# Optimization experiments

Measured on AMD Instinct MI355X. Metric: run time of the kernel, lower is better.

Reference implementation:

```python
import jax, jax.numpy as jnp
import numpy as np

PARTIAL_DATA_THRESHOLD = 0.1  # threshold on squared NN distance (ChamferDistance returns squared dists)


def setup_inputs() -> dict:
    key = jax.random.key(0)
    k1, k2 = jax.random.split(key)
    scan_vertices = jax.random.normal(k1, (50000, 3), dtype=jnp.float32)      # N x 3
    template_vertices = jax.random.normal(k2, (6890, 3), dtype=jnp.float32)   # M x 3
    return {"scan_vertices": scan_vertices, "template_vertices": template_vertices}


def reference(scan_vertices, template_vertices):
    # Directional (template -> scan) Chamfer: for each template point, squared
    # distance to nearest scan point; then sum distances below threshold.
    # d2[m, n] = |t_m|^2 + |s_n|^2 - 2 t_m . s_n
    t_sq = jnp.sum(template_vertices * template_vertices, axis=-1)            # [M]
    s_sq = jnp.sum(scan_vertices * scan_vertices, axis=-1)                    # [N]
    cross = jnp.einsum('md,nd->mn', template_vertices, scan_vertices)         # [M, N]
    d2 = t_sq[:, None] + s_sq[None, :] - 2.0 * cross                          # [M, N]
    template2scan = jnp.min(d2, axis=1)                                       # [M]
    mask = template2scan < PARTIAL_DATA_THRESHOLD
    return jnp.sum(jnp.where(mask, template2scan, 0.0))
```

## Files before the change

### kernel.cpp

```cpp
#include <hip/hip_runtime.h>
#include <hip/hip_bf16.h>

#define BLK 256
#define SPLITS 24
#define FRTOT 1584
#define FPS (FRTOT / SPLITS)
#define NSLOT (FRTOT * 32)
#define THRESH 0.1f
#define KEY_MAX 0xFFFFFFFFu
#define ONE_BF ((unsigned short)0x3F80)

typedef __attribute__((ext_vector_type(8))) short short8;
typedef __attribute__((ext_vector_type(16))) float floatx16;

__device__ __forceinline__ unsigned short f2bf(float x) {
    unsigned u = __float_as_uint(x);
    unsigned r = u + 0x7FFFu + ((u >> 16) & 1u);
    return (unsigned short)(r >> 16);
}
__device__ __forceinline__ float bf2f(unsigned short h) {
    return __uint_as_float(((unsigned)h) << 16);
}

__device__ __forceinline__ unsigned f2key(float f) {
    unsigned b = __float_as_uint(f);
    return (b & 0x80000000u) ? ~b : (b | 0x80000000u);
}
__device__ __forceinline__ float key2f(unsigned k) {
    return __uint_as_float((k & 0x80000000u) ? (k & 0x7FFFFFFFu) : ~k);
}

template <int CTRL>
__device__ __forceinline__ float dpp_ror_min(float v) {
    const int i = __float_as_int(v);
    const int p = __builtin_amdgcn_update_dpp(i, i, CTRL, 0xF, 0xF, false);
    return fminf(v, __int_as_float(p));
}

__global__ __launch_bounds__(BLK) void pdl_prep(const float* __restrict__ scan,
                                                uint4* __restrict__ fragbuf,
                                                unsigned* __restrict__ gmin,
                                                float* __restrict__ out,
                                                int N, int Mpad) {
    const int n = blockIdx.x * BLK + threadIdx.x;
    if (n == 0) out[0] = 0.0f;
    if (n < Mpad) gmin[n] = KEY_MAX;
    if (n >= NSLOT) return;

    unsigned short k[16];
    if (n < N) {
        const float x = scan[3 * n + 0], y = scan[3 * n + 1], z = scan[3 * n + 2];
        const float s2 = fmaf(x, x, fmaf(y, y, z * z));
        const float cx = -2.0f * x, cy = -2.0f * y, cz = -2.0f * z;
        const unsigned short xh = f2bf(cx); const unsigned short xl = f2bf(cx - bf2f(xh));
        const unsigned short yh = f2bf(cy); const unsigned short yl = f2bf(cy - bf2f(yh));
        const unsigned short zh = f2bf(cz); const unsigned short zl = f2bf(cz - bf2f(zh));
        const unsigned short wh = f2bf(s2); const unsigned short wl = f2bf(s2 - bf2f(wh));
        k[0] = xh; k[1] = xl; k[2] = xh; k[3] = xl;
        k[4] = yh; k[5] = yl; k[6] = yh; k[7] = yl;
        k[8] = zh; k[9] = zl; k[10] = zh; k[11] = zl;
        k[12] = ONE_BF; k[13] = ONE_BF;
        k[14] = wh; k[15] = wl;
    } else {
#pragma unroll
        for (int i = 0; i < 16; ++i) k[i] = 0;
        k[12] = ONE_BF; k[13] = ONE_BF;
        k[14] = f2bf(1e30f); k[15] = 0;
    }

    const int g = n >> 5, c = n & 31;
    uint4 lo, hi;
    lo.x = (unsigned)k[0] | ((unsigned)k[1] << 16);
    lo.y = (unsigned)k[2] | ((unsigned)k[3] << 16);
    lo.z = (unsigned)k[4] | ((unsigned)k[5] << 16);
    lo.w = (unsigned)k[6] | ((unsigned)k[7] << 16);
    hi.x = (unsigned)k[8] | ((unsigned)k[9] << 16);
    hi.y = (unsigned)k[10] | ((unsigned)k[11] << 16);
    hi.z = (unsigned)k[12] | ((unsigned)k[13] << 16);
    hi.w = (unsigned)k[14] | ((unsigned)k[15] << 16);
    fragbuf[(size_t)g * 64 + c] = lo;
    fragbuf[(size_t)g * 64 + 32 + c] = hi;
}

__global__ __launch_bounds__(BLK, 4) void pdl_main(const float* __restrict__ tmpl,
                                                   const uint4* __restrict__ fragbuf,
                                                   unsigned* __restrict__ gmin,
                                                   int M) {
    const int tid = threadIdx.x;
    const int wave = tid >> 6, lane = tid & 63;

    const int mbase = (blockIdx.y * 4 + wave) * 32;
    short8 A;
    {
        int m = mbase + (lane & 31);
        if (m > M - 1) m = M - 1;
        const float x = tmpl[3 * m + 0], y = tmpl[3 * m + 1], z = tmpl[3 * m + 2];
        const float t2 = fmaf(x, x, fmaf(y, y, z * z));
        const unsigned short xh = f2bf(x); const unsigned short xl = f2bf(x - bf2f(xh));
        const unsigned short yh = f2bf(y); const unsigned short yl = f2bf(y - bf2f(yh));
        const unsigned short zh = f2bf(z); const unsigned short zl = f2bf(z - bf2f(zh));
        const unsigned short wh = f2bf(t2); const unsigned short wl = f2bf(t2 - bf2f(wh));
        const bool hi = (lane >= 32);
        A[0] = (short)(hi ? zh : xh);
        A[1] = (short)(hi ? zh : xh);
        A[2] = (short)(hi ? zl : xl);
        A[3] = (short)(hi ? zl : xl);
        A[4] = (short)(hi ? wh : yh);
        A[5] = (short)(hi ? wl : yh);
        A[6] = (short)(hi ? ONE_BF : yl);
        A[7] = (short)(hi ? ONE_BF : yl);
    }

    floatx16 mn, zacc;
#pragma unroll
    for (int r = 0; r < 16; ++r) { mn[r] = 3e30f; zacc[r] = 0.0f; }

    const uint4* fb = fragbuf + (size_t)(blockIdx.x * FPS) * 64 + lane;

    union U { uint4 u; short8 s; };
    uint4 p0 = fb[0];
    uint4 p1 = fb[64];
#pragma unroll 1
    for (int f = 0; f < FPS; f += 2) {
        U c0, c1; c0.u = p0; c1.u = p1;
        p0 = fb[(size_t)(f + 2) * 64];
        p1 = fb[(size_t)(f + 3) * 64];
        const floatx16 d0 = __builtin_amdgcn_mfma_f32_32x32x16_bf16(A, c0.s, zacc, 0, 0, 0);
        const floatx16 d1 = __builtin_amdgcn_mfma_f32_32x32x16_bf16(A, c1.s, zacc, 0, 0, 0);
#pragma unroll
        for (int r = 0; r < 16; ++r)
            mn[r] = fminf(fminf(d0[r], d1[r]), mn[r]);
    }

#pragma unroll
    for (int r = 0; r < 16; ++r) {
        float v = mn[r];
        v = dpp_ror_min<0x128>(v);
        v = dpp_ror_min<0x124>(v);
        v = dpp_ror_min<0x122>(v);
        v = dpp_ror_min<0x121>(v);
        const int sw = __builtin_amdgcn_ds_swizzle(__float_as_int(v), 0x401F);
        v = fminf(v, __int_as_float(sw));
        if ((lane & 31) == 0) {
            const int row = (r & 3) + 8 * (r >> 2) + ((lane >> 5) << 2);
            atomicMin(&gmin[mbase + row], f2key(v));
        }
    }
}

__global__ __launch_bounds__(BLK) void pdl_final(const unsigned* __restrict__ gmin,
                                                 float* __restrict__ out, int M) {
    const int m = blockIdx.x * BLK + threadIdx.x;
    float s = 0.0f;
    if (m < M) {
        const float v = key2f(gmin[m]);
        if (v < THRESH) s = v;
    }
#pragma unroll
    for (int off = 32; off > 0; off >>= 1) s += __shfl_down(s, off, 64);

    __shared__ float ls[BLK / 64];
    const int lane = threadIdx.x & 63;
    const int w = threadIdx.x >> 6;
    if (lane == 0) ls[w] = s;
    __syncthreads();
    if (threadIdx.x == 0) {
        float t = 0.0f;
#pragma unroll
        for (int i = 0; i < BLK / 64; ++i) t += ls[i];
        atomicAdd(out, t);
    }
}

extern "C" void kernel_launch(void* const* d_in, const int* in_sizes, int n_in,
                              void* d_out, int out_size, void* d_ws, size_t ws_size,
                              hipStream_t stream) {
    const float* scan = (const float*)d_in[0];
    const float* tmpl = (const float*)d_in[1];
    float* out = (float*)d_out;

    const int N = in_sizes[0] / 3;
    const int M = in_sizes[1] / 3;

    const int tGroups = (M + 127) / 128;
    const int Mpad = ((M + 31) / 32) * 32 + 128;

    unsigned* gmin = (unsigned*)d_ws;
    uint4* fragbuf = (uint4*)((char*)d_ws + 65536);

    pdl_prep<<<(NSLOT + BLK - 1) / BLK, BLK, 0, stream>>>(scan, fragbuf, gmin,
                                                          out, N, Mpad);

    dim3 grid(SPLITS, tGroups);
    pdl_main<<<grid, BLK, 0, stream>>>(tmpl, fragbuf, gmin, M);

    pdl_final<<<(M + BLK - 1) / BLK, BLK, 0, stream>>>(gmin, out, M);
}
```

Measured before the change: 78.15 us.

## Fuse final reduction into main kernel via last-block-done counter, deepen prefetch

```diff
diff --git a/kernel.cpp b/kernel.cpp
--- a/kernel.cpp
+++ b/kernel.cpp
@@ -2,9 +2,9 @@
 #include <hip/hip_bf16.h>
 
 #define BLK 256
-#define SPLITS 24
-#define FRTOT 1584
-#define FPS (FRTOT / SPLITS)
+#define SPLITS 25
+#define FPS 64
+#define FRTOT (SPLITS * FPS)
 #define NSLOT (FRTOT * 32)
 #define THRESH 0.1f
 #define KEY_MAX 0xFFFFFFFFu
@@ -40,10 +40,10 @@
 __global__ __launch_bounds__(BLK) void pdl_prep(const float* __restrict__ scan,
                                                 uint4* __restrict__ fragbuf,
                                                 unsigned* __restrict__ gmin,
-                                                float* __restrict__ out,
+                                                unsigned* __restrict__ done,
                                                 int N, int Mpad) {
     const int n = blockIdx.x * BLK + threadIdx.x;
-    if (n == 0) out[0] = 0.0f;
+    if (n == 0) done[0] = 0u;
     if (n < Mpad) gmin[n] = KEY_MAX;
     if (n >= NSLOT) return;
 
@@ -85,7 +85,9 @@
 __global__ __launch_bounds__(BLK, 4) void pdl_main(const float* __restrict__ tmpl,
                                                    const uint4* __restrict__ fragbuf,
                                                    unsigned* __restrict__ gmin,
-                                                   int M) {
+                                                   unsigned* __restrict__ done,
+                                                   float* __restrict__ out,
+                                                   int M, int nBlocks) {
     const int tid = threadIdx.x;
     const int wave = tid >> 6, lane = tid & 63;
 
@@ -118,18 +120,25 @@
     const uint4* fb = fragbuf + (size_t)(blockIdx.x * FPS) * 64 + lane;
 
     union U { uint4 u; short8 s; };
-    uint4 p0 = fb[0];
-    uint4 p1 = fb[64];
+    uint4 p0 = fb[0 * 64], p1 = fb[1 * 64], p2 = fb[2 * 64], p3 = fb[3 * 64];
 #pragma unroll 1
-    for (int f = 0; f < FPS; f += 2) {
-        U c0, c1; c0.u = p0; c1.u = p1;
-        p0 = fb[(size_t)(f + 2) * 64];
-        p1 = fb[(size_t)(f + 3) * 64];
+    for (int f = 0; f < FPS; f += 4) {
+        U c0, c1, c2, c3;
+        c0.u = p0; c1.u = p1; c2.u = p2; c3.u = p3;
+        p0 = fb[(size_t)(f + 4) * 64];
+        p1 = fb[(size_t)(f + 5) * 64];
+        p2 = fb[(size_t)(f + 6) * 64];
+        p3 = fb[(size_t)(f + 7) * 64];
         const floatx16 d0 = __builtin_amdgcn_mfma_f32_32x32x16_bf16(A, c0.s, zacc, 0, 0, 0);
         const floatx16 d1 = __builtin_amdgcn_mfma_f32_32x32x16_bf16(A, c1.s, zacc, 0, 0, 0);
 #pragma unroll
         for (int r = 0; r < 16; ++r)
             mn[r] = fminf(fminf(d0[r], d1[r]), mn[r]);
+        const floatx16 d2 = __builtin_amdgcn_mfma_f32_32x32x16_bf16(A, c2.s, zacc, 0, 0, 0);
+        const floatx16 d3 = __builtin_amdgcn_mfma_f32_32x32x16_bf16(A, c3.s, zacc, 0, 0, 0);
+#pragma unroll
+        for (int r = 0; r < 16; ++r)
+            mn[r] = fminf(fminf(d2[r], d3[r]), mn[r]);
     }
 
 #pragma unroll
@@ -146,29 +155,28 @@
             atomicMin(&gmin[mbase + row], f2key(v));
         }
     }
-}
-
-__global__ __launch_bounds__(BLK) void pdl_final(const unsigned* __restrict__ gmin,
-                                                 float* __restrict__ out, int M) {
-    const int m = blockIdx.x * BLK + threadIdx.x;
-    float s = 0.0f;
-    if (m < M) {
-        const float v = key2f(gmin[m]);
-        if (v < THRESH) s = v;
-    }
-#pragma unroll
-    for (int off = 32; off > 0; off >>= 1) s += __shfl_down(s, off, 64);
-
+
+    __shared__ unsigned doneRank;
     __shared__ float ls[BLK / 64];
-    const int lane = threadIdx.x & 63;
-    const int w = threadIdx.x >> 6;
-    if (lane == 0) ls[w] = s;
+    __threadfence();
+    if (tid == 0) doneRank = atomicAdd(done, 1u);
     __syncthreads();
-    if (threadIdx.x == 0) {
-        float t = 0.0f;
-#pragma unroll
-        for (int i = 0; i < BLK / 64; ++i) t += ls[i];
-        atomicAdd(out, t);
+    if (doneRank == (unsigned)(nBlocks - 1)) {
+        float s = 0.0f;
+        for (int m = tid; m < M; m += BLK) {
+            const float v = key2f(atomicMin(&gmin[m], KEY_MAX));
+            if (v < THRESH) s += v;
+        }
+#pragma unroll
+        for (int off = 32; off > 0; off >>= 1) s += __shfl_down(s, off, 64);
+        if (lane == 0) ls[wave] = s;
+        __syncthreads();
+        if (tid == 0) {
+            float t = 0.0f;
+#pragma unroll
+            for (int i = 0; i < BLK / 64; ++i) t += ls[i];
+            out[0] = t;
+        }
     }
 }
 
@@ -183,16 +191,16 @@
     const int M = in_sizes[1] / 3;
 
     const int tGroups = (M + 127) / 128;
-    const int Mpad = ((M + 31) / 32) * 32 + 128;
+    const int Mpad = tGroups * 128;
 
     unsigned* gmin = (unsigned*)d_ws;
+    unsigned* done = (unsigned*)((char*)d_ws + 32768);
     uint4* fragbuf = (uint4*)((char*)d_ws + 65536);
 
     pdl_prep<<<(NSLOT + BLK - 1) / BLK, BLK, 0, stream>>>(scan, fragbuf, gmin,
-                                                          out, N, Mpad);
+                                                          done, N, Mpad);
 
     dim3 grid(SPLITS, tGroups);
-    pdl_main<<<grid, BLK, 0, stream>>>(tmpl, fragbuf, gmin, M);
-
-    pdl_final<<<(M + BLK - 1) / BLK, BLK, 0, stream>>>(gmin, out, M);
-}
+    pdl_main<<<grid, BLK, 0, stream>>>(tmpl, fragbuf, gmin, done, out, M,
+                                       SPLITS * tGroups);
+}
```

After: 161.6 us. +106.8%, slower.

## Process two template fragments per wave to reuse each scan fragment load

Applied to the files above, without the earlier changes.

```diff
diff --git a/kernel.cpp b/kernel.cpp
--- a/kernel.cpp
+++ b/kernel.cpp
@@ -2,9 +2,9 @@
 #include <hip/hip_bf16.h>
 
 #define BLK 256
-#define SPLITS 24
-#define FRTOT 1584
-#define FPS (FRTOT / SPLITS)
+#define SPLITS 25
+#define FPS 64
+#define FRTOT (SPLITS * FPS)
 #define NSLOT (FRTOT * 32)
 #define THRESH 0.1f
 #define KEY_MAX 0xFFFFFFFFu
@@ -89,10 +89,11 @@
     const int tid = threadIdx.x;
     const int wave = tid >> 6, lane = tid & 63;
 
-    const int mbase = (blockIdx.y * 4 + wave) * 32;
-    short8 A;
-    {
-        int m = mbase + (lane & 31);
+    const int mbase = (blockIdx.y * 4 + wave) * 64;
+    short8 A0, A1;
+#pragma unroll
+    for (int af = 0; af < 2; ++af) {
+        int m = mbase + af * 32 + (lane & 31);
         if (m > M - 1) m = M - 1;
         const float x = tmpl[3 * m + 0], y = tmpl[3 * m + 1], z = tmpl[3 * m + 2];
         const float t2 = fmaf(x, x, fmaf(y, y, z * z));
@@ -101,49 +102,58 @@
         const unsigned short zh = f2bf(z); const unsigned short zl = f2bf(z - bf2f(zh));
         const unsigned short wh = f2bf(t2); const unsigned short wl = f2bf(t2 - bf2f(wh));
         const bool hi = (lane >= 32);
-        A[0] = (short)(hi ? zh : xh);
-        A[1] = (short)(hi ? zh : xh);
-        A[2] = (short)(hi ? zl : xl);
-        A[3] = (short)(hi ? zl : xl);
-        A[4] = (short)(hi ? wh : yh);
-        A[5] = (short)(hi ? wl : yh);
-        A[6] = (short)(hi ? ONE_BF : yl);
-        A[7] = (short)(hi ? ONE_BF : yl);
-    }
-
-    floatx16 mn, zacc;
-#pragma unroll
-    for (int r = 0; r < 16; ++r) { mn[r] = 3e30f; zacc[r] = 0.0f; }
+        short8 a;
+        a[0] = (short)(hi ? zh : xh);
+        a[1] = (short)(hi ? zh : xh);
+        a[2] = (short)(hi ? zl : xl);
+        a[3] = (short)(hi ? zl : xl);
+        a[4] = (short)(hi ? wh : yh);
+        a[5] = (short)(hi ? wl : yh);
+        a[6] = (short)(hi ? ONE_BF : yl);
+        a[7] = (short)(hi ? ONE_BF : yl);
+        if (af == 0) A0 = a; else A1 = a;
+    }
+
+    floatx16 mn0, mn1, zacc;
+#pragma unroll
+    for (int r = 0; r < 16; ++r) { mn0[r] = 3e30f; mn1[r] = 3e30f; zacc[r] = 0.0f; }
 
     const uint4* fb = fragbuf + (size_t)(blockIdx.x * FPS) * 64 + lane;
 
     union U { uint4 u; short8 s; };
-    uint4 p0 = fb[0];
-    uint4 p1 = fb[64];
+    uint4 p0 = fb[0 * 64], p1 = fb[1 * 64];
 #pragma unroll 1
     for (int f = 0; f < FPS; f += 2) {
-        U c0, c1; c0.u = p0; c1.u = p1;
+        U c0, c1;
+        c0.u = p0; c1.u = p1;
         p0 = fb[(size_t)(f + 2) * 64];
         p1 = fb[(size_t)(f + 3) * 64];
-        const floatx16 d0 = __builtin_amdgcn_mfma_f32_32x32x16_bf16(A, c0.s, zacc, 0, 0, 0);
-        const floatx16 d1 = __builtin_amdgcn_mfma_f32_32x32x16_bf16(A, c1.s, zacc, 0, 0, 0);
-#pragma unroll
-        for (int r = 0; r < 16; ++r)
-            mn[r] = fminf(fminf(d0[r], d1[r]), mn[r]);
-    }
-
-#pragma unroll
-    for (int r = 0; r < 16; ++r) {
-        float v = mn[r];
-        v = dpp_ror_min<0x128>(v);
-        v = dpp_ror_min<0x124>(v);
-        v = dpp_ror_min<0x122>(v);
-        v = dpp_ror_min<0x121>(v);
-        const int sw = __builtin_amdgcn_ds_swizzle(__float_as_int(v), 0x401F);
-        v = fminf(v, __int_as_float(sw));
-        if ((lane & 31) == 0) {
-            const int row = (r & 3) + 8 * (r >> 2) + ((lane >> 5) << 2);
-            atomicMin(&gmin[mbase + row], f2key(v));
+        const floatx16 d00 = __builtin_amdgcn_mfma_f32_32x32x16_bf16(A0, c0.s, zacc, 0, 0, 0);
+        const floatx16 d10 = __builtin_amdgcn_mfma_f32_32x32x16_bf16(A1, c0.s, zacc, 0, 0, 0);
+        const floatx16 d01 = __builtin_amdgcn_mfma_f32_32x32x16_bf16(A0, c1.s, zacc, 0, 0, 0);
+        const floatx16 d11 = __builtin_amdgcn_mfma_f32_32x32x16_bf16(A1, c1.s, zacc, 0, 0, 0);
+#pragma unroll
+        for (int r = 0; r < 16; ++r) {
+            mn0[r] = fminf(fminf(d00[r], d01[r]), mn0[r]);
+            mn1[r] = fminf(fminf(d10[r], d11[r]), mn1[r]);
+        }
+    }
+
+#pragma unroll
+    for (int af = 0; af < 2; ++af) {
+#pragma unroll
+        for (int r = 0; r < 16; ++r) {
+            float v = (af == 0) ? mn0[r] : mn1[r];
+            v = dpp_ror_min<0x128>(v);
+            v = dpp_ror_min<0x124>(v);
+            v = dpp_ror_min<0x122>(v);
+            v = dpp_ror_min<0x121>(v);
+            const int sw = __builtin_amdgcn_ds_swizzle(__float_as_int(v), 0x401F);
+            v = fminf(v, __int_as_float(sw));
+            if ((lane & 31) == 0) {
+                const int row = (r & 3) + 8 * (r >> 2) + ((lane >> 5) << 2);
+                atomicMin(&gmin[mbase + af * 32 + row], f2key(v));
+            }
         }
     }
 }
@@ -182,8 +192,8 @@
     const int N = in_sizes[0] / 3;
     const int M = in_sizes[1] / 3;
 
-    const int tGroups = (M + 127) / 128;
-    const int Mpad = ((M + 31) / 32) * 32 + 128;
+    const int tGroups = (M + 255) / 256;
+    const int Mpad = tGroups * 256;
 
     unsigned* gmin = (unsigned*)d_ws;
     uint4* fragbuf = (uint4*)((char*)d_ws + 65536);
```

Result: slower. 81.04 us (+3.7%).
